# Optimization experiments

Measured on AMD Instinct MI355X. Metric: run time of the kernel, lower is better.

The kernel has to match this reference:

```python
import jax, jax.numpy as jnp
import numpy as np

EPS = 1e-5

def _bn(x, mean, var, gamma, beta, axis=1):
    # eval-mode BatchNorm over channel `axis`
    shape = [1] * x.ndim
    shape[axis] = x.shape[axis]
    r = lambda a: a.reshape(shape)
    return (x - r(mean)) * jax.lax.rsqrt(r(var) + EPS) * r(gamma) + r(beta)

def _forward(hs_init, adjs0, adjs1, adjs2, W_init, W0, W1, W2, W3, b,
             fc1_w, fc1_b,
             bn_init_mean, bn_init_var, bn_init_gamma, bn_init_beta,
             bn_layer_mean, bn_layer_var, bn_layer_gamma, bn_layer_beta,
             bn_graph_mean, bn_graph_var, bn_graph_gamma, bn_graph_beta):
    L = W0.shape[0]
    adjs = adjs0 + adjs1 + adjs2                      # [B,N,N]
    conn, c0, c1, c2 = [adjs], [adjs0], [adjs1], [adjs2]
    # h[0]: [B,N,F]
    h = [jax.nn.relu(_bn(jnp.matmul(hs_init, W_init),
                         bn_init_mean, bn_init_var, bn_init_gamma, bn_init_beta, axis=1))]
    for l in range(L):
        h_tmp = jnp.matmul(h[l], W3[l]) + b[l]
        for i in range(l + 1):
            h_tmp = h_tmp \
                + jnp.matmul(jnp.matmul(c0[i], h[l - i]), W0[l]) \
                + jnp.matmul(jnp.matmul(c1[i], h[l - i]), W1[l]) \
                + jnp.matmul(jnp.matmul(c2[i], h[l - i]), W2[l])
        h.append(jax.nn.relu(_bn(h_tmp, bn_layer_mean[l], bn_layer_var[l],
                                 bn_layer_gamma[l], bn_layer_beta[l], axis=1)))
        conn.append(jnp.matmul(conn[l], adjs))
        c0.append(jnp.matmul(conn[l], adjs0))
        c1.append(jnp.matmul(conn[l], adjs1))
        c2.append(jnp.matmul(conn[l], adjs2))
    sum_result = jnp.sum(h[L], axis=1)                # [B,F]
    graph_h = jax.nn.relu(_bn(sum_result, bn_graph_mean, bn_graph_var,
                              bn_graph_gamma, bn_graph_beta, axis=1))
    # dropout is identity in eval mode
    logits = jnp.matmul(graph_h, fc1_w.T) + fc1_b     # [B,A]
    return jax.nn.softmax(logits, axis=1)             # exp(log_softmax) == softmax

def setup_inputs() -> dict:
    B, N, F, L, A = 16, 512, 64, 3, 512
    key = jax.random.key(0)
    ks = jax.random.split(key, 26)
    d = {}
    d['hs_init'] = jax.random.normal(ks[0], (B, N, N), jnp.float32)
    d['adjs0'] = jax.random.uniform(ks[1], (B, N, N), jnp.float32)
    d['adjs1'] = jax.random.uniform(ks[2], (B, N, N), jnp.float32)
    d['adjs2'] = jax.random.uniform(ks[3], (B, N, N), jnp.float32)
    d['W_init'] = jax.random.normal(ks[4], (N, F), jnp.float32) * 0.05
    d['W0'] = jax.random.normal(ks[5], (L, F, F), jnp.float32) * 0.02
    d['W1'] = jax.random.normal(ks[6], (L, F, F), jnp.float32) * 0.02
    d['W2'] = jax.random.normal(ks[7], (L, F, F), jnp.float32) * 0.02
    d['W3'] = jax.random.normal(ks[8], (L, F, F), jnp.float32) * 0.02
    d['b'] = jax.random.normal(ks[9], (L, F), jnp.float32)
    d['fc1_w'] = jax.random.normal(ks[10], (A, F), jnp.float32) * 0.05
    d['fc1_b'] = jax.random.normal(ks[11], (A,), jnp.float32) * 0.05
    d['bn_init_mean'] = jax.random.normal(ks[12], (N,), jnp.float32)
    d['bn_init_var'] = jax.random.uniform(ks[13], (N,), jnp.float32) + 0.5
    d['bn_init_gamma'] = jax.random.normal(ks[14], (N,), jnp.float32) * 0.1 + 1.0
    d['bn_init_beta'] = jax.random.normal(ks[15], (N,), jnp.float32) * 0.1
    d['bn_layer_mean'] = jax.random.normal(ks[16], (L, N), jnp.float32)
    d['bn_layer_var'] = jax.random.uniform(ks[17], (L, N), jnp.float32) + 0.5
    d['bn_layer_gamma'] = jax.random.normal(ks[18], (L, N), jnp.float32) * 0.1 + 1.0
    d['bn_layer_beta'] = jax.random.normal(ks[19], (L, N), jnp.float32) * 0.1
    d['bn_graph_mean'] = jax.random.normal(ks[20], (F,), jnp.float32)
    d['bn_graph_var'] = jax.random.uniform(ks[21], (F,), jnp.float32) + 0.5
    d['bn_graph_gamma'] = jax.random.normal(ks[22], (F,), jnp.float32) * 0.1 + 1.0
    d['bn_graph_beta'] = jax.random.normal(ks[23], (F,), jnp.float32) * 0.1
    return d

def reference(hs_init, adjs0, adjs1, adjs2, W_init, W0, W1, W2, W3, b,
              fc1_w, fc1_b,
              bn_init_mean, bn_init_var, bn_init_gamma, bn_init_beta,
              bn_layer_mean, bn_layer_var, bn_layer_gamma, bn_layer_beta,
              bn_graph_mean, bn_graph_var, bn_graph_gamma, bn_graph_beta):
    return _forward(hs_init, adjs0, adjs1, adjs2, W_init, W0, W1, W2, W3, b,
                    fc1_w, fc1_b,
                    bn_init_mean, bn_init_var, bn_init_gamma, bn_init_beta,
                    bn_layer_mean, bn_layer_var, bn_layer_gamma, bn_layer_beta,
                    bn_graph_mean, bn_graph_var, bn_graph_gamma, bn_graph_beta)
```

## Files before the change

### kernel.cpp

```cpp
#include <hip/hip_runtime.h>

typedef __attribute__((ext_vector_type(8))) short bf16x8;
typedef __attribute__((ext_vector_type(4))) float f32x4;
typedef __attribute__((ext_vector_type(8))) unsigned short u16x8;

constexpr int Bn = 16;
constexpr int Nn = 512;
constexpr int Fn = 64;
constexpr int Aout = 512;

static __device__ __forceinline__ unsigned short f2bf(float f) {
  union { float f; unsigned int u; } v; v.f = f;
  unsigned int r = v.u + 0x7fffu + ((v.u >> 16) & 1u);
  return (unsigned short)(r >> 16);
}
static __device__ __forceinline__ float bf2f(unsigned short u) {
  union { unsigned int u; float f; } v; v.u = ((unsigned int)u) << 16;
  return v.f;
}
static __device__ __forceinline__ unsigned int pk2(float a, float b) {
  union { float f; unsigned int u; } ua, ub; ua.f = a; ub.f = b;
  return ((ua.u + 0x8000u) >> 16) | ((ub.u + 0x8000u) & 0xFFFF0000u);
}
static __device__ __forceinline__ void gload_lds16(const float* g, float* l) {
  __builtin_amdgcn_global_load_lds(
      (const __attribute__((address_space(1))) void*)g,
      (__attribute__((address_space(3))) void*)l, 16, 0, 0);
}


__launch_bounds__(256)
__global__ void prep_kernel(const float* __restrict__ Wi,
                            unsigned short* __restrict__ Wp,
                            const float* __restrict__ W0,
                            const float* __restrict__ W1,
                            const float* __restrict__ W2,
                            const float* __restrict__ W3,
                            unsigned short* __restrict__ Wall) {
  const int blk = blockIdx.x;
  if (blk < 16) {
    const int idx = blk * 256 + threadIdx.x;
    const int f = idx >> 6, o = idx & 63;
    const int k0 = o * 8;
    const size_t dst = ((size_t)((f >> 4) * 16 + (k0 >> 5)) << 9) +
                       (((f & 15) + 16 * ((k0 >> 3) & 3)) << 3);
    unsigned short w[8];
#pragma unroll
    for (int j = 0; j < 8; ++j) w[j] = f2bf(Wi[(size_t)(k0 + j) * Fn + f]);
    *(uint4*)(Wp + dst) = *(const uint4*)w;
  } else {
    const int r = blk - 16;
    const int mat = r >> 1;
    const int l = mat >> 2, m = mat & 3;
    const int idx = (r & 1) * 256 + threadIdx.x;
    const int co = idx >> 3, oct = idx & 7;
    const int k0 = oct * 8;
    const float* src = (m == 0 ? W3 : m == 1 ? W0 : m == 2 ? W1 : W2) + l * 4096;
    const size_t dst = (size_t)mat * 4096 +
                       ((size_t)((co >> 4) * 2 + (k0 >> 5)) << 9) +
                       (((co & 15) + 16 * ((k0 >> 3) & 3)) << 3);
    unsigned short w[8];
#pragma unroll
    for (int j = 0; j < 8; ++j) w[j] = f2bf(src[(k0 + j) * 64 + co]);
    *(uint4*)(Wall + dst) = *(const uint4*)w;
  }
}

__launch_bounds__(256, 1)
__global__ void h0_kernel(const float* __restrict__ hs,
                          const unsigned short* __restrict__ Wp,
                          const float* __restrict__ mean,
                          const float* __restrict__ var,
                          const float* __restrict__ gamma,
                          const float* __restrict__ beta,
                          unsigned short* __restrict__ operm,
                          unsigned short* __restrict__ olin) {
  const int b = blockIdx.y;
  const int R0 = blockIdx.x * 32;
  const int tid = threadIdx.x;
  const int w = tid >> 6, l = tid & 63;
  const int lr = l & 15, q = l >> 4;
  const int nsub = (w & 1) * 16;
  const int cstart = (w >> 1) * 2;

  const float* Af =
      hs + ((size_t)b << 18) + (size_t)(R0 + nsub + lr) * 512 + q * 8;
  const unsigned short* Xf = Wp + cstart * 8192 + l * 8;

  f32x4 acc[2] = {{0.f, 0.f, 0.f, 0.f}, {0.f, 0.f, 0.f, 0.f}};
  float4 ral[2][2];
  bf16x8 xb[2][2];
#define LD0(S_, T_)                                                       \
  {                                                                       \
    ral[S_][0] = *(const float4*)(Af + (T_)*32);                          \
    ral[S_][1] = *(const float4*)(Af + (T_)*32 + 4);                      \
    xb[S_][0] = *(const bf16x8*)(Xf + (T_)*512);                          \
    xb[S_][1] = *(const bf16x8*)(Xf + 8192 + (T_)*512);                   \
  }
  LD0(0, 0)
#pragma unroll
  for (int t = 0; t < 16; ++t) {
    const int cur = t & 1;
    if (t + 1 < 16) LD0(cur ^ 1, t + 1)
    union { bf16x8 v; unsigned int u[4]; } cv;
    cv.u[0] = pk2(ral[cur][0].x, ral[cur][0].y);
    cv.u[1] = pk2(ral[cur][0].z, ral[cur][0].w);
    cv.u[2] = pk2(ral[cur][1].x, ral[cur][1].y);
    cv.u[3] = pk2(ral[cur][1].z, ral[cur][1].w);
#pragma unroll
    for (int c = 0; c < 2; ++c)
      acc[c] = __builtin_amdgcn_mfma_f32_16x16x32_bf16(cv.v, xb[cur][c], acc[c], 0, 0, 0);
  }
#undef LD0

  __shared__ __align__(16) unsigned short Tfn[64][40];
  __shared__ __align__(16) unsigned short Tnf[32][72];
  float sc[4], mu[4], bt[4];
#pragma unroll
  for (int i = 0; i < 4; ++i) {
    int n = R0 + nsub + q * 4 + i;
    sc[i] = rsqrtf(var[n] + 1e-5f) * gamma[n];
    mu[i] = mean[n];
    bt[i] = beta[n];
  }
#pragma unroll
  for (int c = 0; c < 2; ++c) {
    const int f = (cstart + c) * 16 + lr;
    ushort4 wv;
#pragma unroll
    for (int i = 0; i < 4; ++i) {
      float v = fmaxf(fmaf(acc[c][i] - mu[i], sc[i], bt[i]), 0.f);
      unsigned short uv = f2bf(v);
      ((unsigned short*)&wv)[i] = uv;
      Tnf[nsub + q * 4 + i][f] = uv;
    }
    *(ushort4*)&Tfn[f][nsub + q * 4] = wv;
  }
  __syncthreads();
  {
    const int f = tid >> 2, oc = tid & 3;
    const int n = R0 + oc * 8;
    const size_t dst = ((size_t)b << 15) +
                       ((size_t)((f >> 4) * 16 + (n >> 5)) << 9) +
                       (((f & 15) + 16 * ((n >> 3) & 3)) << 3);
    *(uint4*)(operm + dst) = *(const uint4*)&Tfn[f][oc * 8];
    const int nl = tid >> 3, oc8 = tid & 7;
    *(uint4*)(olin + ((size_t)b << 15) + (size_t)(R0 + nl) * 64 + oc8 * 8) =
        *(const uint4*)&Tnf[nl][oc8 * 8];
  }
}

struct LArgs {
  const float* Af0;
  const float* Af1;
  const float* Af2;
  const unsigned short* Xh;
  const unsigned short* XP[3];
  const unsigned short* hlin;
  const unsigned short* Wl;
  const float *bias, *mean, *var, *gamma, *beta;
  unsigned short* hperm_o;
  unsigned short* hlin_o;
  unsigned short* Po[3];
};

template <int NSEG>
__launch_bounds__(256, 2)
__global__ void layer_kernel(LArgs La) {
  const int flat = blockIdx.x;
  const int b = (flat & 7) + 8 * ((flat >> 3) & 1);
  const int R0 = (flat >> 4) * 16;
  const int tid = threadIdx.x;
  const int w = tid >> 6, l = tid & 63;
  const int lr = l & 15, q = l >> 4;

  __shared__ __align__(16) float Asg[2][3][16][64];
  __shared__ __align__(16) unsigned short Tnf[3][16][72];
  __shared__ __align__(16) unsigned short Tfn[3][64][24];
  __shared__ __align__(16) unsigned short Hfn[64][24];
  __shared__ __align__(16) unsigned short Hnf[16][72];

  const float* Az = (w == 0) ? La.Af0 : (w == 1) ? La.Af1 : La.Af2;
  const float* Abase = Az + ((size_t)b << 18) + (size_t)R0 * 512;
  size_t aoff[4];
#pragma unroll
  for (int c = 0; c < 4; ++c) {
    const int arow = c * 4 + (l >> 4);
    const int agc = (l & 15) ^ arow;
    aoff[c] = (size_t)arow * 512 + agc * 4;
  }

  const size_t xoff = ((size_t)b << 15) + (size_t)w * 8192 + l * 8;
  const unsigned short* Xhp = La.Xh + xoff;
  const unsigned short* XP0p = (NSEG == 2) ? La.XP[0] + xoff : Xhp;
  const unsigned short* XP1p = (NSEG == 2) ? La.XP[1] + xoff : Xhp;
  const unsigned short* XP2p = (NSEG == 2) ? La.XP[2] + xoff : Xhp;

  f32x4 acc[3] = {{0.f, 0.f, 0.f, 0.f},
                  {0.f, 0.f, 0.f, 0.f},
                  {0.f, 0.f, 0.f, 0.f}};
  bf16x8 rxh[2][2];
  bf16x8 rxp[2][3][2];

#define STAGE(BB, T)                                                     \
  if (w < 3) {                                                           \
    _Pragma("unroll") for (int c = 0; c < 4; ++c)                        \
        gload_lds16(Abase + aoff[c] + (T)*64, &Asg[BB][w][c * 4][0]);    \
  }
#define LOADX(S_, T_)                                                    \
  {                                                                      \
    rxh[S_][0] = *(const bf16x8*)(Xhp + (2 * (T_)) * 512);               \
    rxh[S_][1] = *(const bf16x8*)(Xhp + (2 * (T_) + 1) * 512);           \
    if (NSEG == 2) {                                                     \
      rxp[S_][0][0] = *(const bf16x8*)(XP0p + (2 * (T_)) * 512);         \
      rxp[S_][0][1] = *(const bf16x8*)(XP0p + (2 * (T_) + 1) * 512);     \
      rxp[S_][1][0] = *(const bf16x8*)(XP1p + (2 * (T_)) * 512);         \
      rxp[S_][1][1] = *(const bf16x8*)(XP1p + (2 * (T_) + 1) * 512);     \
      rxp[S_][2][0] = *(const bf16x8*)(XP2p + (2 * (T_)) * 512);         \
      rxp[S_][2][1] = *(const bf16x8*)(XP2p + (2 * (T_) + 1) * 512);     \
    }                                                                    \
  }

  STAGE(0, 0)
  LOADX(0, 0)
  __syncthreads();

#pragma unroll
  for (int t = 0; t < 8; ++t) {
    const int cur = t & 1;
    if (t + 1 < 8) {
      STAGE(cur ^ 1, t + 1)
      LOADX(cur ^ 1, t + 1)
    }
#pragma unroll
    for (int kf = 0; kf < 2; ++kf) {
      float4 fa[3], fb[3];
#pragma unroll
      for (int z = 0; z < 3; ++z) {
        fa[z] = *(const float4*)&Asg[cur][z][lr][((kf * 8 + 2 * q) ^ lr) << 2];
        fb[z] = *(const float4*)&Asg[cur][z][lr][((kf * 8 + 2 * q + 1) ^ lr) << 2];
      }
      bf16x8 azf[3];
#pragma unroll
      for (int z = 0; z < 3; ++z) {
        union { bf16x8 v; unsigned int u[4]; } cv;
        cv.u[0] = pk2(fa[z].x, fa[z].y);
        cv.u[1] = pk2(fa[z].z, fa[z].w);
        cv.u[2] = pk2(fb[z].x, fb[z].y);
        cv.u[3] = pk2(fb[z].z, fb[z].w);
        azf[z] = cv.v;
      }
      bf16x8 asumf;
      if (NSEG == 2) {
        union { bf16x8 v; unsigned int u[4]; } cv;
        cv.u[0] = pk2(fa[0].x + fa[1].x + fa[2].x, fa[0].y + fa[1].y + fa[2].y);
        cv.u[1] = pk2(fa[0].z + fa[1].z + fa[2].z, fa[0].w + fa[1].w + fa[2].w);
        cv.u[2] = pk2(fb[0].x + fb[1].x + fb[2].x, fb[0].y + fb[1].y + fb[2].y);
        cv.u[3] = pk2(fb[0].z + fb[1].z + fb[2].z, fb[0].w + fb[1].w + fb[2].w);
        asumf = cv.v;
      }
#pragma unroll
      for (int z = 0; z < 3; ++z) {
        acc[z] = __builtin_amdgcn_mfma_f32_16x16x32_bf16(azf[z], rxh[cur][kf],
                                                         acc[z], 0, 0, 0);
        if (NSEG == 2)
          acc[z] = __builtin_amdgcn_mfma_f32_16x16x32_bf16(
              asumf, rxp[cur][z][kf], acc[z], 0, 0, 0);
      }
    }
    __syncthreads();
  }
#undef STAGE
#undef LOADX

#pragma unroll
  for (int z = 0; z < 3; ++z) {
    const int f = w * 16 + lr;
    ushort4 wv;
#pragma unroll
    for (int i = 0; i < 4; ++i) {
      unsigned short uv = f2bf(acc[z][i]);
      ((unsigned short*)&wv)[i] = uv;
      Tnf[z][q * 4 + i][f] = uv;
    }
    *(ushort4*)&Tfn[z][f][q * 4] = wv;
  }
  __syncthreads();

  if (La.Po[0] != nullptr && tid < 128) {
    const int f = tid >> 1, o = tid & 1;
    const int n = R0 + o * 8;
    const size_t dst = ((size_t)b << 15) +
                       ((size_t)((f >> 4) * 16 + (n >> 5)) << 9) +
                       (((f & 15) + 16 * ((n >> 3) & 3)) << 3);
#pragma unroll
    for (int z = 0; z < 3; ++z)
      *(uint4*)(La.Po[z] + dst) = *(const uint4*)&Tfn[z][f][o * 8];
  }

  f32x4 acch = {0.f, 0.f, 0.f, 0.f};
#pragma unroll
  for (int m = 0; m < 4; ++m) {
#pragma unroll
    for (int ks = 0; ks < 2; ++ks) {
      bf16x8 af;
      if (m == 0)
        af = *(const bf16x8*)(La.hlin + ((size_t)b << 15) +
                              (size_t)(R0 + lr) * 64 + q * 8 + ks * 32);
      else
        af = *(const bf16x8*)&Tnf[m - 1][lr][q * 8 + ks * 32];
      const bf16x8 bf_ = *(const bf16x8*)(La.Wl + m * 4096 +
                                          ((size_t)(w * 2 + ks) << 9) + l * 8);
      acch = __builtin_amdgcn_mfma_f32_16x16x32_bf16(af, bf_, acch, 0, 0, 0);
    }
  }

  {
    float sc[4], mu[4], bt[4];
#pragma unroll
    for (int i = 0; i < 4; ++i) {
      int n = R0 + q * 4 + i;
      sc[i] = rsqrtf(La.var[n] + 1e-5f) * La.gamma[n];
      mu[i] = La.mean[n];
      bt[i] = La.beta[n];
    }
    const int f = w * 16 + lr;
    const float bia = La.bias[f];
    ushort4 wv;
#pragma unroll
    for (int i = 0; i < 4; ++i) {
      float v = acch[i] + bia;
      v = fmaxf(fmaf(v - mu[i], sc[i], bt[i]), 0.f);
      unsigned short uv = f2bf(v);
      ((unsigned short*)&wv)[i] = uv;
      Hnf[q * 4 + i][f] = uv;
    }
    *(ushort4*)&Hfn[f][q * 4] = wv;
  }
  __syncthreads();

  if (tid < 128) {
    const int f = tid >> 1, o = tid & 1;
    const int n = R0 + o * 8;
    const size_t dst = ((size_t)b << 15) +
                       ((size_t)((f >> 4) * 16 + (n >> 5)) << 9) +
                       (((f & 15) + 16 * ((n >> 3) & 3)) << 3);
    *(uint4*)(La.hperm_o + dst) = *(const uint4*)&Hfn[f][o * 8];
    if (La.hlin_o != nullptr) {
      const int nl = tid >> 3, oc8 = tid & 7;
      *(uint4*)(La.hlin_o + ((size_t)b << 15) + (size_t)(R0 + nl) * 64 +
                oc8 * 8) = *(const uint4*)&Hnf[nl][oc8 * 8];
    }
  }
}

__launch_bounds__(256)
__global__ void head_kernel(const unsigned short* __restrict__ h3p,
                            const float* __restrict__ gmean,
                            const float* __restrict__ gvar,
                            const float* __restrict__ ggamma,
                            const float* __restrict__ gbeta,
                            const float* __restrict__ fc_w,
                            const float* __restrict__ fc_b,
                            float* __restrict__ out) {
  const int b = blockIdx.x;
  const int t = threadIdx.x;
  __shared__ float part[256];
  __shared__ float gh[64];
  __shared__ float red[256];

  const int f = t >> 2, q = t & 3;
  const unsigned short* hp = h3p + ((size_t)b << 15);
  float s = 0.f;
#pragma unroll
  for (int m = 0; m < 16; ++m) {
    const int n = q * 128 + m * 8;
    const size_t off = ((size_t)((f >> 4) * 16 + (n >> 5)) << 9) +
                       (((f & 15) + 16 * ((n >> 3) & 3)) << 3);
    u16x8 v = *(const u16x8*)(hp + off);
#pragma unroll
    for (int e = 0; e < 8; ++e) s += bf2f((unsigned short)v[e]);
  }
  part[t] = s;
  __syncthreads();
  if (t < 64) {
    float sum = part[t * 4] + part[t * 4 + 1] + part[t * 4 + 2] + part[t * 4 + 3];
    float sc = rsqrtf(gvar[t] + 1e-5f) * ggamma[t];
    float v = fmaf(sum - gmean[t], sc, gbeta[t]);
    gh[t] = v > 0.f ? v : 0.f;
  }
  __syncthreads();

  float lg[2];
#pragma unroll
  for (int rep = 0; rep < 2; ++rep) {
    const int a = t + rep * 256;
    const float* __restrict__ wv = fc_w + (size_t)a * Fn;
    float acc = fc_b[a];
#pragma unroll 8
    for (int kk = 0; kk < 64; ++kk) acc = fmaf(gh[kk], wv[kk], acc);
    lg[rep] = acc;
  }
  red[t] = fmaxf(lg[0], lg[1]);
  __syncthreads();
  for (int off = 128; off > 0; off >>= 1) {
    if (t < off) red[t] = fmaxf(red[t], red[t + off]);
    __syncthreads();
  }
  const float mx = red[0];
  __syncthreads();
  const float e0 = __expf(lg[0] - mx), e1 = __expf(lg[1] - mx);
  red[t] = e0 + e1;
  __syncthreads();
  for (int off = 128; off > 0; off >>= 1) {
    if (t < off) red[t] += red[t + off];
    __syncthreads();
  }
  const float inv = 1.f / red[0];
  out[(size_t)b * Aout + t] = e0 * inv;
  out[(size_t)b * Aout + t + 256] = e1 * inv;
}

extern "C" void kernel_launch(void* const* d_in, const int* in_sizes, int n_in,
                              void* d_out, int out_size, void* d_ws,
                              size_t ws_size, hipStream_t stream) {
  (void)in_sizes; (void)n_in; (void)out_size; (void)ws_size;
  const float* hs_init = (const float*)d_in[0];
  const float* adjs0 = (const float*)d_in[1];
  const float* adjs1 = (const float*)d_in[2];
  const float* adjs2 = (const float*)d_in[3];
  const float* W_init = (const float*)d_in[4];
  const float* W0 = (const float*)d_in[5];
  const float* W1 = (const float*)d_in[6];
  const float* W2 = (const float*)d_in[7];
  const float* W3 = (const float*)d_in[8];
  const float* bvec = (const float*)d_in[9];
  const float* fc1_w = (const float*)d_in[10];
  const float* fc1_b = (const float*)d_in[11];
  const float* bn_init_mean = (const float*)d_in[12];
  const float* bn_init_var = (const float*)d_in[13];
  const float* bn_init_gamma = (const float*)d_in[14];
  const float* bn_init_beta = (const float*)d_in[15];
  const float* bn_layer_mean = (const float*)d_in[16];
  const float* bn_layer_var = (const float*)d_in[17];
  const float* bn_layer_gamma = (const float*)d_in[18];
  const float* bn_layer_beta = (const float*)d_in[19];
  const float* bn_graph_mean = (const float*)d_in[20];
  const float* bn_graph_var = (const float*)d_in[21];
  const float* bn_graph_gamma = (const float*)d_in[22];
  const float* bn_graph_beta = (const float*)d_in[23];

  const size_t NF = (size_t)Bn * Fn * Nn;

  unsigned short* wsu = (unsigned short*)d_ws;
  unsigned short* Wp = wsu;
  unsigned short* Wall = Wp + 32768;
  unsigned short* hApe = Wall + 49152;
  unsigned short* hBpe = hApe + NF;
  unsigned short* hAli = hBpe + NF;
  unsigned short* hBli = hAli + NF;
  unsigned short* PA0 = hBli + NF;
  unsigned short* PA1 = PA0 + NF;
  unsigned short* PA2 = PA1 + NF;
  unsigned short* PB0 = PA2 + NF;
  unsigned short* PB1 = PB0 + NF;
  unsigned short* PB2 = PB1 + NF;

  prep_kernel<<<dim3(40), dim3(256), 0, stream>>>(W_init, Wp, W0, W1, W2, W3,
                                                  Wall);

  h0_kernel<<<dim3(16, Bn), dim3(256), 0, stream>>>(
      hs_init, Wp, bn_init_mean, bn_init_var, bn_init_gamma, bn_init_beta,
      hApe, hAli);

  {
    LArgs La = {};
    La.Af0 = adjs0; La.Af1 = adjs1; La.Af2 = adjs2;
    La.Xh = hApe; La.hlin = hAli;
    La.Wl = Wall;
    La.bias = bvec; La.mean = bn_layer_mean; La.var = bn_layer_var;
    La.gamma = bn_layer_gamma; La.beta = bn_layer_beta;
    La.hperm_o = hBpe; La.hlin_o = hBli;
    La.Po[0] = PA0; La.Po[1] = PA1; La.Po[2] = PA2;
    layer_kernel<1><<<dim3(512), dim3(256), 0, stream>>>(La);
  }
  {
    LArgs La = {};
    La.Af0 = adjs0; La.Af1 = adjs1; La.Af2 = adjs2;
    La.Xh = hBpe; La.hlin = hBli;
    La.XP[0] = PA0; La.XP[1] = PA1; La.XP[2] = PA2;
    La.Wl = Wall + 4 * 4096;
    La.bias = bvec + 64; La.mean = bn_layer_mean + 512;
    La.var = bn_layer_var + 512; La.gamma = bn_layer_gamma + 512;
    La.beta = bn_layer_beta + 512;
    La.hperm_o = hApe; La.hlin_o = hAli;
    La.Po[0] = PB0; La.Po[1] = PB1; La.Po[2] = PB2;
    layer_kernel<2><<<dim3(512), dim3(256), 0, stream>>>(La);
  }
  {
    LArgs La = {};
    La.Af0 = adjs0; La.Af1 = adjs1; La.Af2 = adjs2;
    La.Xh = hApe; La.hlin = hAli;
    La.XP[0] = PB0; La.XP[1] = PB1; La.XP[2] = PB2;
    La.Wl = Wall + 8 * 4096;
    La.bias = bvec + 128; La.mean = bn_layer_mean + 1024;
    La.var = bn_layer_var + 1024; La.gamma = bn_layer_gamma + 1024;
    La.beta = bn_layer_beta + 1024;
    La.hperm_o = hBpe; La.hlin_o = nullptr;
    La.Po[0] = nullptr; La.Po[1] = nullptr; La.Po[2] = nullptr;
    layer_kernel<2><<<dim3(512), dim3(256), 0, stream>>>(La);
  }

  head_kernel<<<dim3(Bn), dim3(256), 0, stream>>>(
      hBpe, bn_graph_mean, bn_graph_var, bn_graph_gamma, bn_graph_beta, fc1_w,
      fc1_b, (float*)d_out);
}
```

Before: 68.55 us.

## Cache bf16 adjacency and summed adjacency from layer 0 for later layers

The first layer kernel now also writes bf16 copies of the three adjacency matrices and their elementwise sum to workspace while it streams them. Later layers read these bf16 copies directly into MFMA operands from global memory, with no LDS staging, fp32-to-bf16 conversion or summing. This cuts per-layer adjacency read bytes and the ALU/LDS work. In exchange, layer 0 takes on extra global writes and the workspace grows by four adjacency-sized buffers.

```diff
diff --git a/kernel.cpp b/kernel.cpp
--- a/kernel.cpp
+++ b/kernel.cpp
@@ -150,10 +150,205 @@
   }
 }
 
-struct LArgs {
+struct L0Args {
   const float* Af0;
   const float* Af1;
   const float* Af2;
+  const unsigned short* Xh;
+  const unsigned short* hlin;
+  const unsigned short* Wl;
+  const float *bias, *mean, *var, *gamma, *beta;
+  unsigned short* hperm_o;
+  unsigned short* hlin_o;
+  unsigned short* Po[3];
+  unsigned short* ab0;
+  unsigned short* ab1;
+  unsigned short* ab2;
+  unsigned short* absum;
+};
+
+__launch_bounds__(256, 2)
+__global__ void layer0_kernel(L0Args La) {
+  const int flat = blockIdx.x;
+  const int b = (flat & 7) + 8 * ((flat >> 3) & 1);
+  const int R0 = (flat >> 4) * 16;
+  const int tid = threadIdx.x;
+  const int w = tid >> 6, l = tid & 63;
+  const int lr = l & 15, q = l >> 4;
+
+  __shared__ __align__(16) float Asg[2][3][16][64];
+  __shared__ __align__(16) unsigned short Tnf[3][16][72];
+  __shared__ __align__(16) unsigned short Tfn[3][64][24];
+  __shared__ __align__(16) unsigned short Hfn[64][24];
+  __shared__ __align__(16) unsigned short Hnf[16][72];
+
+  const float* Az = (w == 0) ? La.Af0 : (w == 1) ? La.Af1 : La.Af2;
+  const float* Abase = Az + ((size_t)b << 18) + (size_t)R0 * 512;
+  size_t aoff[4];
+#pragma unroll
+  for (int c = 0; c < 4; ++c) {
+    const int arow = c * 4 + (l >> 4);
+    const int agc = (l & 15) ^ arow;
+    aoff[c] = (size_t)arow * 512 + agc * 4;
+  }
+
+  const size_t xoff = ((size_t)b << 15) + (size_t)w * 8192 + l * 8;
+  const unsigned short* Xhp = La.Xh + xoff;
+
+  f32x4 acc[3] = {{0.f, 0.f, 0.f, 0.f},
+                  {0.f, 0.f, 0.f, 0.f},
+                  {0.f, 0.f, 0.f, 0.f}};
+  bf16x8 rxh[2][2];
+
+#define STAGE(BB, T)                                                     \
+  if (w < 3) {                                                           \
+    _Pragma("unroll") for (int c = 0; c < 4; ++c)                        \
+        gload_lds16(Abase + aoff[c] + (T)*64, &Asg[BB][w][c * 4][0]);    \
+  }
+#define LOADX(S_, T_)                                                    \
+  {                                                                      \
+    rxh[S_][0] = *(const bf16x8*)(Xhp + (2 * (T_)) * 512);               \
+    rxh[S_][1] = *(const bf16x8*)(Xhp + (2 * (T_) + 1) * 512);           \
+  }
+
+  STAGE(0, 0)
+  LOADX(0, 0)
+  __syncthreads();
+
+  const int er = tid >> 4, esc = tid & 15, egc = esc ^ er;
+
+#pragma unroll
+  for (int t = 0; t < 8; ++t) {
+    const int cur = t & 1;
+    if (t + 1 < 8) {
+      STAGE(cur ^ 1, t + 1)
+      LOADX(cur ^ 1, t + 1)
+    }
+#pragma unroll
+    for (int kf = 0; kf < 2; ++kf) {
+      float4 fa[3], fb[3];
+#pragma unroll
+      for (int z = 0; z < 3; ++z) {
+        fa[z] = *(const float4*)&Asg[cur][z][lr][((kf * 8 + 2 * q) ^ lr) << 2];
+        fb[z] = *(const float4*)&Asg[cur][z][lr][((kf * 8 + 2 * q + 1) ^ lr) << 2];
+      }
+#pragma unroll
+      for (int z = 0; z < 3; ++z) {
+        union { bf16x8 v; unsigned int u[4]; } cv;
+        cv.u[0] = pk2(fa[z].x, fa[z].y);
+        cv.u[1] = pk2(fa[z].z, fa[z].w);
+        cv.u[2] = pk2(fb[z].x, fb[z].y);
+        cv.u[3] = pk2(fb[z].z, fb[z].w);
+        acc[z] = __builtin_amdgcn_mfma_f32_16x16x32_bf16(cv.v, rxh[cur][kf],
+                                                         acc[z], 0, 0, 0);
+      }
+    }
+    {
+      float4 v0 = *(const float4*)&Asg[cur][0][er][esc * 4];
+      float4 v1 = *(const float4*)&Asg[cur][1][er][esc * 4];
+      float4 v2 = *(const float4*)&Asg[cur][2][er][esc * 4];
+      const size_t go =
+          ((size_t)b << 18) + (size_t)(R0 + er) * 512 + t * 64 + egc * 4;
+      uint2 wv;
+      wv.x = pk2(v0.x, v0.y); wv.y = pk2(v0.z, v0.w);
+      *(uint2*)(La.ab0 + go) = wv;
+      wv.x = pk2(v1.x, v1.y); wv.y = pk2(v1.z, v1.w);
+      *(uint2*)(La.ab1 + go) = wv;
+      wv.x = pk2(v2.x, v2.y); wv.y = pk2(v2.z, v2.w);
+      *(uint2*)(La.ab2 + go) = wv;
+      wv.x = pk2(v0.x + v1.x + v2.x, v0.y + v1.y + v2.y);
+      wv.y = pk2(v0.z + v1.z + v2.z, v0.w + v1.w + v2.w);
+      *(uint2*)(La.absum + go) = wv;
+    }
+    __syncthreads();
+  }
+#undef STAGE
+#undef LOADX
+
+#pragma unroll
+  for (int z = 0; z < 3; ++z) {
+    const int f = w * 16 + lr;
+    ushort4 wv;
+#pragma unroll
+    for (int i = 0; i < 4; ++i) {
+      unsigned short uv = f2bf(acc[z][i]);
+      ((unsigned short*)&wv)[i] = uv;
+      Tnf[z][q * 4 + i][f] = uv;
+    }
+    *(ushort4*)&Tfn[z][f][q * 4] = wv;
+  }
+  __syncthreads();
+
+  if (tid < 128) {
+    const int f = tid >> 1, o = tid & 1;
+    const int n = R0 + o * 8;
+    const size_t dst = ((size_t)b << 15) +
+                       ((size_t)((f >> 4) * 16 + (n >> 5)) << 9) +
+                       (((f & 15) + 16 * ((n >> 3) & 3)) << 3);
+#pragma unroll
+    for (int z = 0; z < 3; ++z)
+      *(uint4*)(La.Po[z] + dst) = *(const uint4*)&Tfn[z][f][o * 8];
+  }
+
+  f32x4 acch = {0.f, 0.f, 0.f, 0.f};
+#pragma unroll
+  for (int m = 0; m < 4; ++m) {
+#pragma unroll
+    for (int ks = 0; ks < 2; ++ks) {
+      bf16x8 af;
+      if (m == 0)
+        af = *(const bf16x8*)(La.hlin + ((size_t)b << 15) +
+                              (size_t)(R0 + lr) * 64 + q * 8 + ks * 32);
+      else
+        af = *(const bf16x8*)&Tnf[m - 1][lr][q * 8 + ks * 32];
+      const bf16x8 bf_ = *(const bf16x8*)(La.Wl + m * 4096 +
+                                          ((size_t)(w * 2 + ks) << 9) + l * 8);
+      acch = __builtin_amdgcn_mfma_f32_16x16x32_bf16(af, bf_, acch, 0, 0, 0);
+    }
+  }
+
+  {
+    float sc[4], mu[4], bt[4];
+#pragma unroll
+    for (int i = 0; i < 4; ++i) {
+      int n = R0 + q * 4 + i;
+      sc[i] = rsqrtf(La.var[n] + 1e-5f) * La.gamma[n];
+      mu[i] = La.mean[n];
+      bt[i] = La.beta[n];
+    }
+    const int f = w * 16 + lr;
+    const float bia = La.bias[f];
+    ushort4 wv;
+#pragma unroll
+    for (int i = 0; i < 4; ++i) {
+      float v = acch[i] + bia;
+      v = fmaxf(fmaf(v - mu[i], sc[i], bt[i]), 0.f);
+      unsigned short uv = f2bf(v);
+      ((unsigned short*)&wv)[i] = uv;
+      Hnf[q * 4 + i][f] = uv;
+    }
+    *(ushort4*)&Hfn[f][q * 4] = wv;
+  }
+  __syncthreads();
+
+  if (tid < 128) {
+    const int f = tid >> 1, o = tid & 1;
+    const int n = R0 + o * 8;
+    const size_t dst = ((size_t)b << 15) +
+                       ((size_t)((f >> 4) * 16 + (n >> 5)) << 9) +
+                       (((f & 15) + 16 * ((n >> 3) & 3)) << 3);
+    *(uint4*)(La.hperm_o + dst) = *(const uint4*)&Hfn[f][o * 8];
+    const int nl = tid >> 3, oc8 = tid & 7;
+    *(uint4*)(La.hlin_o + ((size_t)b << 15) + (size_t)(R0 + nl) * 64 +
+              oc8 * 8) = *(const uint4*)&Hnf[nl][oc8 * 8];
+  }
+}
+
+struct LNArgs {
+  const unsigned short* ab0;
+  const unsigned short* ab1;
+  const unsigned short* ab2;
+  const unsigned short* absum;
   const unsigned short* Xh;
   const unsigned short* XP[3];
   const unsigned short* hlin;
@@ -164,9 +359,8 @@
   unsigned short* Po[3];
 };
 
-template <int NSEG>
 __launch_bounds__(256, 2)
-__global__ void layer_kernel(LArgs La) {
+__global__ void layerN_kernel(LNArgs La) {
   const int flat = blockIdx.x;
   const int b = (flat & 7) + 8 * ((flat >> 3) & 1);
   const int R0 = (flat >> 4) * 16;
@@ -174,104 +368,54 @@
   const int w = tid >> 6, l = tid & 63;
   const int lr = l & 15, q = l >> 4;
 
-  __shared__ __align__(16) float Asg[2][3][16][64];
   __shared__ __align__(16) unsigned short Tnf[3][16][72];
   __shared__ __align__(16) unsigned short Tfn[3][64][24];
   __shared__ __align__(16) unsigned short Hfn[64][24];
   __shared__ __align__(16) unsigned short Hnf[16][72];
 
-  const float* Az = (w == 0) ? La.Af0 : (w == 1) ? La.Af1 : La.Af2;
-  const float* Abase = Az + ((size_t)b << 18) + (size_t)R0 * 512;
-  size_t aoff[4];
-#pragma unroll
-  for (int c = 0; c < 4; ++c) {
-    const int arow = c * 4 + (l >> 4);
-    const int agc = (l & 15) ^ arow;
-    aoff[c] = (size_t)arow * 512 + agc * 4;
-  }
-
+  const size_t aoff = ((size_t)b << 18) + (size_t)(R0 + lr) * 512 + q * 8;
+  const unsigned short* A0 = La.ab0 + aoff;
+  const unsigned short* A1 = La.ab1 + aoff;
+  const unsigned short* A2 = La.ab2 + aoff;
+  const unsigned short* AS = La.absum + aoff;
   const size_t xoff = ((size_t)b << 15) + (size_t)w * 8192 + l * 8;
-  const unsigned short* Xhp = La.Xh + xoff;
-  const unsigned short* XP0p = (NSEG == 2) ? La.XP[0] + xoff : Xhp;
-  const unsigned short* XP1p = (NSEG == 2) ? La.XP[1] + xoff : Xhp;
-  const unsigned short* XP2p = (NSEG == 2) ? La.XP[2] + xoff : Xhp;
+  const unsigned short* XH = La.Xh + xoff;
+  const unsigned short* X0 = La.XP[0] + xoff;
+  const unsigned short* X1 = La.XP[1] + xoff;
+  const unsigned short* X2 = La.XP[2] + xoff;
 
   f32x4 acc[3] = {{0.f, 0.f, 0.f, 0.f},
                   {0.f, 0.f, 0.f, 0.f},
                   {0.f, 0.f, 0.f, 0.f}};
-  bf16x8 rxh[2][2];
-  bf16x8 rxp[2][3][2];
-
-#define STAGE(BB, T)                                                     \
-  if (w < 3) {                                                           \
-    _Pragma("unroll") for (int c = 0; c < 4; ++c)                        \
-        gload_lds16(Abase + aoff[c] + (T)*64, &Asg[BB][w][c * 4][0]);    \
-  }
-#define LOADX(S_, T_)                                                    \
-  {                                                                      \
-    rxh[S_][0] = *(const bf16x8*)(Xhp + (2 * (T_)) * 512);               \
-    rxh[S_][1] = *(const bf16x8*)(Xhp + (2 * (T_) + 1) * 512);           \
-    if (NSEG == 2) {                                                     \
-      rxp[S_][0][0] = *(const bf16x8*)(XP0p + (2 * (T_)) * 512);         \
-      rxp[S_][0][1] = *(const bf16x8*)(XP0p + (2 * (T_) + 1) * 512);     \
-      rxp[S_][1][0] = *(const bf16x8*)(XP1p + (2 * (T_)) * 512);         \
-      rxp[S_][1][1] = *(const bf16x8*)(XP1p + (2 * (T_) + 1) * 512);     \
-      rxp[S_][2][0] = *(const bf16x8*)(XP2p + (2 * (T_)) * 512);         \
-      rxp[S_][2][1] = *(const bf16x8*)(XP2p + (2 * (T_) + 1) * 512);     \
-    }                                                                    \
-  }
-
-  STAGE(0, 0)
-  LOADX(0, 0)
-  __syncthreads();
-
-#pragma unroll
-  for (int t = 0; t < 8; ++t) {
+  bf16x8 ra[2][4], rx[2][4];
+
+#define LDN(S_, T_)                                          \
+  {                                                          \
+    ra[S_][0] = *(const bf16x8*)(A0 + (T_)*32);              \
+    ra[S_][1] = *(const bf16x8*)(A1 + (T_)*32);              \
+    ra[S_][2] = *(const bf16x8*)(A2 + (T_)*32);              \
+    ra[S_][3] = *(const bf16x8*)(AS + (T_)*32);              \
+    rx[S_][0] = *(const bf16x8*)(XH + (T_)*512);             \
+    rx[S_][1] = *(const bf16x8*)(X0 + (T_)*512);             \
+    rx[S_][2] = *(const bf16x8*)(X1 + (T_)*512);             \
+    rx[S_][3] = *(const bf16x8*)(X2 + (T_)*512);             \
+  }
+
+  LDN(0, 0)
+#pragma unroll
+  for (int t = 0; t < 16; ++t) {
     const int cur = t & 1;
-    if (t + 1 < 8) {
-      STAGE(cur ^ 1, t + 1)
-      LOADX(cur ^ 1, t + 1)
-    }
-#pragma unroll
-    for (int kf = 0; kf < 2; ++kf) {
-      float4 fa[3], fb[3];
-#pragma unroll
-      for (int z = 0; z < 3; ++z) {
-        fa[z] = *(const float4*)&Asg[cur][z][lr][((kf * 8 + 2 * q) ^ lr) << 2];
-        fb[z] = *(const float4*)&Asg[cur][z][lr][((kf * 8 + 2 * q + 1) ^ lr) << 2];
-      }
-      bf16x8 azf[3];
-#pragma unroll
-      for (int z = 0; z < 3; ++z) {
-        union { bf16x8 v; unsigned int u[4]; } cv;
-        cv.u[0] = pk2(fa[z].x, fa[z].y);
-        cv.u[1] = pk2(fa[z].z, fa[z].w);
-        cv.u[2] = pk2(fb[z].x, fb[z].y);
-        cv.u[3] = pk2(fb[z].z, fb[z].w);
-        azf[z] = cv.v;
-      }
-      bf16x8 asumf;
-      if (NSEG == 2) {
-        union { bf16x8 v; unsigned int u[4]; } cv;
-        cv.u[0] = pk2(fa[0].x + fa[1].x + fa[2].x, fa[0].y + fa[1].y + fa[2].y);
-        cv.u[1] = pk2(fa[0].z + fa[1].z + fa[2].z, fa[0].w + fa[1].w + fa[2].w);
-        cv.u[2] = pk2(fb[0].x + fb[1].x + fb[2].x, fb[0].y + fb[1].y + fb[2].y);
-        cv.u[3] = pk2(fb[0].z + fb[1].z + fb[2].z, fb[0].w + fb[1].w + fb[2].w);
-        asumf = cv.v;
-      }
-#pragma unroll
-      for (int z = 0; z < 3; ++z) {
-        acc[z] = __builtin_amdgcn_mfma_f32_16x16x32_bf16(azf[z], rxh[cur][kf],
-                                                         acc[z], 0, 0, 0);
-        if (NSEG == 2)
-          acc[z] = __builtin_amdgcn_mfma_f32_16x16x32_bf16(
-              asumf, rxp[cur][z][kf], acc[z], 0, 0, 0);
-      }
-    }
-    __syncthreads();
-  }
-#undef STAGE
-#undef LOADX
+    if (t + 1 < 16) LDN(cur ^ 1, t + 1)
+#pragma unroll
+    for (int z = 0; z < 3; ++z) {
+      acc[z] = __builtin_amdgcn_mfma_f32_16x16x32_bf16(ra[cur][z], rx[cur][0],
+                                                       acc[z], 0, 0, 0);
+      acc[z] = __builtin_amdgcn_mfma_f32_16x16x32_bf16(ra[cur][3],
+                                                       rx[cur][z + 1], acc[z],
+                                                       0, 0, 0);
+    }
+  }
+#undef LDN
 
 #pragma unroll
   for (int z = 0; z < 3; ++z) {
@@ -451,6 +595,7 @@
   const float* bn_graph_beta = (const float*)d_in[23];
 
   const size_t NF = (size_t)Bn * Fn * Nn;
+  const size_t ADJ = (size_t)Bn * Nn * Nn;
 
   unsigned short* wsu = (unsigned short*)d_ws;
   unsigned short* Wp = wsu;
@@ -465,6 +610,10 @@
   unsigned short* PB0 = PA2 + NF;
   unsigned short* PB1 = PB0 + NF;
   unsigned short* PB2 = PB1 + NF;
+  unsigned short* ab0 = PB2 + NF;
+  unsigned short* ab1 = ab0 + ADJ;
+  unsigned short* ab2 = ab1 + ADJ;
+  unsigned short* absum = ab2 + ADJ;
 
   prep_kernel<<<dim3(40), dim3(256), 0, stream>>>(W_init, Wp, W0, W1, W2, W3,
                                                   Wall);
@@ -474,7 +623,7 @@
       hApe, hAli);
 
   {
-    LArgs La = {};
+    L0Args La = {};
     La.Af0 = adjs0; La.Af1 = adjs1; La.Af2 = adjs2;
     La.Xh = hApe; La.hlin = hAli;
     La.Wl = Wall;
@@ -482,11 +631,12 @@
     La.gamma = bn_layer_gamma; La.beta = bn_layer_beta;
     La.hperm_o = hBpe; La.hlin_o = hBli;
     La.Po[0] = PA0; La.Po[1] = PA1; La.Po[2] = PA2;
-    layer_kernel<1><<<dim3(512), dim3(256), 0, stream>>>(La);
+    La.ab0 = ab0; La.ab1 = ab1; La.ab2 = ab2; La.absum = absum;
+    layer0_kernel<<<dim3(512), dim3(256), 0, stream>>>(La);
   }
   {
-    LArgs La = {};
-    La.Af0 = adjs0; La.Af1 = adjs1; La.Af2 = adjs2;
+    LNArgs La = {};
+    La.ab0 = ab0; La.ab1 = ab1; La.ab2 = ab2; La.absum = absum;
     La.Xh = hBpe; La.hlin = hBli;
     La.XP[0] = PA0; La.XP[1] = PA1; La.XP[2] = PA2;
     La.Wl = Wall + 4 * 4096;
@@ -495,11 +645,11 @@
     La.beta = bn_layer_beta + 512;
     La.hperm_o = hApe; La.hlin_o = hAli;
     La.Po[0] = PB0; La.Po[1] = PB1; La.Po[2] = PB2;
-    layer_kernel<2><<<dim3(512), dim3(256), 0, stream>>>(La);
+    layerN_kernel<<<dim3(512), dim3(256), 0, stream>>>(La);
   }
   {
-    LArgs La = {};
-    La.Af0 = adjs0; La.Af1 = adjs1; La.Af2 = adjs2;
+    LNArgs La = {};
+    La.ab0 = ab0; La.ab1 = ab1; La.ab2 = ab2; La.absum = absum;
     La.Xh = hApe; La.hlin = hAli;
     La.XP[0] = PB0; La.XP[1] = PB1; La.XP[2] = PB2;
     La.Wl = Wall + 8 * 4096;
@@ -508,7 +658,7 @@
     La.beta = bn_layer_beta + 1024;
     La.hperm_o = hBpe; La.hlin_o = nullptr;
     La.Po[0] = nullptr; La.Po[1] = nullptr; La.Po[2] = nullptr;
-    layer_kernel<2><<<dim3(512), dim3(256), 0, stream>>>(La);
+    layerN_kernel<<<dim3(512), dim3(256), 0, stream>>>(La);
   }
 
   head_kernel<<<dim3(Bn), dim3(256), 0, stream>>>(
```

Result: slower. 85.23 us (+24.3%).

## Stage 128-wide A tiles and pipeline X fragment loads per k-fragment

Applied to the files above, without the earlier changes.

Doubles the LDS A-staging tile from 64 to 128 columns, halving the number of outer K iterations and __syncthreads barriers (8 to 4). X operand register prefetch is restructured to load one fragment ahead per 32-wide k step instead of a whole tile ahead, which cuts register pressure. The cost is more LDS per block (Asg grows from 24KB to 48KB), which may reduce occupancy under the 2-blocks-per-CU launch bound.

```diff
diff --git a/kernel.cpp b/kernel.cpp
--- a/kernel.cpp
+++ b/kernel.cpp
@@ -174,7 +174,7 @@
   const int w = tid >> 6, l = tid & 63;
   const int lr = l & 15, q = l >> 4;
 
-  __shared__ __align__(16) float Asg[2][3][16][64];
+  __shared__ __align__(16) float Asg[2][3][16][128];
   __shared__ __align__(16) unsigned short Tnf[3][16][72];
   __shared__ __align__(16) unsigned short Tfn[3][64][24];
   __shared__ __align__(16) unsigned short Hfn[64][24];
@@ -182,12 +182,14 @@
 
   const float* Az = (w == 0) ? La.Af0 : (w == 1) ? La.Af1 : La.Af2;
   const float* Abase = Az + ((size_t)b << 18) + (size_t)R0 * 512;
-  size_t aoff[4];
-#pragma unroll
-  for (int c = 0; c < 4; ++c) {
-    const int arow = c * 4 + (l >> 4);
-    const int agc = (l & 15) ^ arow;
-    aoff[c] = (size_t)arow * 512 + agc * 4;
+  size_t aoff[8];
+#pragma unroll
+  for (int c = 0; c < 8; ++c) {
+    const int flat_s = c * 64 + l;
+    const int srow = flat_s >> 5;
+    const int schunk = flat_s & 31;
+    const int gchunk = schunk ^ srow;
+    aoff[c] = (size_t)srow * 512 + gchunk * 4;
   }
 
   const size_t xoff = ((size_t)b << 15) + (size_t)w * 8192 + l * 8;
@@ -199,46 +201,44 @@
   f32x4 acc[3] = {{0.f, 0.f, 0.f, 0.f},
                   {0.f, 0.f, 0.f, 0.f},
                   {0.f, 0.f, 0.f, 0.f}};
-  bf16x8 rxh[2][2];
-  bf16x8 rxp[2][3][2];
+  bf16x8 rxh[2];
+  bf16x8 rxp[2][3];
 
 #define STAGE(BB, T)                                                     \
   if (w < 3) {                                                           \
-    _Pragma("unroll") for (int c = 0; c < 4; ++c)                        \
-        gload_lds16(Abase + aoff[c] + (T)*64, &Asg[BB][w][c * 4][0]);    \
-  }
-#define LOADX(S_, T_)                                                    \
+    float* dst_ = (float*)Asg[BB][w];                                    \
+    _Pragma("unroll") for (int c = 0; c < 8; ++c)                        \
+        gload_lds16(Abase + aoff[c] + (T)*128, dst_ + c * 256);          \
+  }
+#define LOADXF(S_, FT_)                                                  \
   {                                                                      \
-    rxh[S_][0] = *(const bf16x8*)(Xhp + (2 * (T_)) * 512);               \
-    rxh[S_][1] = *(const bf16x8*)(Xhp + (2 * (T_) + 1) * 512);           \
+    rxh[S_] = *(const bf16x8*)(Xhp + (FT_)*512);                         \
     if (NSEG == 2) {                                                     \
-      rxp[S_][0][0] = *(const bf16x8*)(XP0p + (2 * (T_)) * 512);         \
-      rxp[S_][0][1] = *(const bf16x8*)(XP0p + (2 * (T_) + 1) * 512);     \
-      rxp[S_][1][0] = *(const bf16x8*)(XP1p + (2 * (T_)) * 512);         \
-      rxp[S_][1][1] = *(const bf16x8*)(XP1p + (2 * (T_) + 1) * 512);     \
-      rxp[S_][2][0] = *(const bf16x8*)(XP2p + (2 * (T_)) * 512);         \
-      rxp[S_][2][1] = *(const bf16x8*)(XP2p + (2 * (T_) + 1) * 512);     \
+      rxp[S_][0] = *(const bf16x8*)(XP0p + (FT_)*512);                   \
+      rxp[S_][1] = *(const bf16x8*)(XP1p + (FT_)*512);                   \
+      rxp[S_][2] = *(const bf16x8*)(XP2p + (FT_)*512);                   \
     }                                                                    \
   }
 
   STAGE(0, 0)
-  LOADX(0, 0)
-  __syncthreads();
-
-#pragma unroll
-  for (int t = 0; t < 8; ++t) {
+  LOADXF(0, 0)
+  __syncthreads();
+
+#pragma unroll
+  for (int t = 0; t < 4; ++t) {
     const int cur = t & 1;
-    if (t + 1 < 8) {
-      STAGE(cur ^ 1, t + 1)
-      LOADX(cur ^ 1, t + 1)
-    }
-#pragma unroll
-    for (int kf = 0; kf < 2; ++kf) {
+    if (t + 1 < 4) STAGE(cur ^ 1, t + 1)
+#pragma unroll
+    for (int kf = 0; kf < 4; ++kf) {
+      const int ft = t * 4 + kf;
+      const int xc = ft & 1;
+      if (ft + 1 < 16) LOADXF(xc ^ 1, ft + 1)
       float4 fa[3], fb[3];
 #pragma unroll
       for (int z = 0; z < 3; ++z) {
         fa[z] = *(const float4*)&Asg[cur][z][lr][((kf * 8 + 2 * q) ^ lr) << 2];
-        fb[z] = *(const float4*)&Asg[cur][z][lr][((kf * 8 + 2 * q + 1) ^ lr) << 2];
+        fb[z] =
+            *(const float4*)&Asg[cur][z][lr][((kf * 8 + 2 * q + 1) ^ lr) << 2];
       }
       bf16x8 azf[3];
 #pragma unroll
@@ -261,17 +261,17 @@
       }
 #pragma unroll
       for (int z = 0; z < 3; ++z) {
-        acc[z] = __builtin_amdgcn_mfma_f32_16x16x32_bf16(azf[z], rxh[cur][kf],
+        acc[z] = __builtin_amdgcn_mfma_f32_16x16x32_bf16(azf[z], rxh[xc],
                                                          acc[z], 0, 0, 0);
         if (NSEG == 2)
-          acc[z] = __builtin_amdgcn_mfma_f32_16x16x32_bf16(
-              asumf, rxp[cur][z][kf], acc[z], 0, 0, 0);
+          acc[z] = __builtin_amdgcn_mfma_f32_16x16x32_bf16(asumf, rxp[xc][z],
+                                                           acc[z], 0, 0, 0);
       }
     }
     __syncthreads();
   }
 #undef STAGE
-#undef LOADX
+#undef LOADXF
 
 #pragma unroll
   for (int z = 0; z < 3; ++z) {
```

Result: slower. 70.91 us (+3.4%).
